# Kernel optimization log

Hardware: AMD Instinct MI355X
Metric: run time of the kernel (lower is better)

## Reference

```python
import jax, jax.numpy as jnp
import numpy as np

# Matches init_kwargs: pc_range=[-54,-54,-5,54,54,3], voxel_size=[0.2,0.2,1.0]
PC_LO = jnp.array([-54.0, -54.0, -5.0], jnp.float32)
PC_HI = jnp.array([54.0, 54.0, 3.0], jnp.float32)
VOX = jnp.array([0.2, 0.2, 1.0], jnp.float32)
NX, NY, NZ = 540, 540, 8          # round((hi-lo)/voxel_size), x,y,z order
NV = NX * NY * NZ                  # dense voxel count (2,332,800)


def setup_inputs() -> dict:
    key = jax.random.key(0)
    B, N = 4, 300000
    k1, k2 = jax.random.split(key)
    center = (PC_LO + PC_HI) / 2.0
    half = (PC_HI - PC_LO) / 2.0 * 1.05
    xyz = center + (jax.random.uniform(k1, (B, N, 3), jnp.float32) * 2.0 - 1.0) * half
    feats = jax.random.normal(k2, (B, N, 2), jnp.float32)
    points = jnp.concatenate([xyz, feats], axis=-1)  # [B, N, 5]
    return {"points": points}


def reference(points):
    """Dynamic voxelization: range filter + quantize + scatter-mean per voxel.

    torch's data-dependent `unique` + compaction is not jit-shapeable, so the
    per-voxel means are returned on the dense [NV, F] grid (occupied voxels are
    those with counts > 0); the math per occupied voxel is identical to the
    original scatter_mean over unique coords.
    """
    grid_max = jnp.array([NX - 1, NY - 1, NZ - 1], jnp.int32)

    def voxelize(pts):  # pts: [N, 5]
        xyz = pts[:, :3]
        keep = jnp.all((xyz >= PC_LO) & (xyz <= PC_HI), axis=1)  # [N]
        # coords in (z, y, x) order in the original; compute (x,y,z) then linearize as z-major
        c = jnp.floor((xyz - PC_LO) / VOX).astype(jnp.int32)
        c = jnp.clip(c, 0, grid_max)  # boundary points (x == hi) map to last cell
        lin = (c[:, 2] * NY + c[:, 1]) * NX + c[:, 0]  # [N]
        lin = jnp.where(keep, lin, NV)  # dropped points -> dummy segment
        pts_m = jnp.where(keep[:, None], pts, 0.0)
        sums = jax.ops.segment_sum(pts_m, lin, num_segments=NV + 1)[:NV]            # [NV, 5]
        cnts = jax.ops.segment_sum(keep.astype(pts.dtype), lin, num_segments=NV + 1)[:NV]  # [NV]
        means = sums / jnp.maximum(cnts, 1.0)[:, None]
        return means, cnts

    voxels, counts = jax.vmap(voxelize)(points)  # [B, NV, 5], [B, NV]
    shape_np = jnp.array([NX, NY, NZ], jnp.int32)
    return voxels, counts, shape_np
```

## Files before the change

kernel.cpp:

```cpp
#include <hip/hip_runtime.h>


#define NX_ 540
#define NY_ 540
#define NZ_ 8
#define NV_ (NX_ * NY_ * NZ_)
#define B_ 4
#define N_ 300000
#define BN_ (B_ * N_)
#define NVB_ (B_ * NV_)


__global__ __launch_bounds__(256) void voxel_build(
    const float* __restrict__ pts,
    int* __restrict__ head,
    int* __restrict__ nxt)
{
    int g = blockIdx.x * blockDim.x + threadIdx.x;
    if (g >= BN_) return;

    const float* p = pts + (size_t)g * 5;
    float x = p[0];
    float y = p[1];
    float z = p[2];

    bool keep = (x >= -54.0f) & (x <= 54.0f) &
                (y >= -54.0f) & (y <= 54.0f) &
                (z >= -5.0f)  & (z <= 3.0f);
    if (!keep) return;

    int cx = (int)floorf((x + 54.0f) * 5.0f);
    int cy = (int)floorf((y + 54.0f) * 5.0f);
    int cz = (int)floorf(z + 5.0f);
    cx = min(max(cx, 0), NX_ - 1);
    cy = min(max(cy, 0), NY_ - 1);
    cz = min(max(cz, 0), NZ_ - 1);

    int lin = (cz * NY_ + cy) * NX_ + cx;
    int b = g / N_;
    int vox = b * NV_ + lin;

    int old = atomicExch(&head[vox], g);
    nxt[g] = old;
}


__global__ __launch_bounds__(256) void voxel_output4(
    const int* __restrict__ head,
    const int* __restrict__ nxt,
    const float* __restrict__ pts,
    float* __restrict__ means,
    float* __restrict__ cnts,
    float* __restrict__ shape_out)
{
    int t = blockIdx.x * blockDim.x + threadIdx.x;
    if (t == 0) {
        shape_out[0] = 540.0f;
        shape_out[1] = 540.0f;
        shape_out[2] = 8.0f;
    }
    int v0 = t * 4;
    if (v0 >= NVB_) return;

    int4 h4 = *(const int4*)(head + v0);
    int hh[4] = {h4.x, h4.y, h4.z, h4.w};

    float o[20];
    float cf[4];

    #pragma unroll
    for (int j = 0; j < 4; j++) {
        int i = hh[j];
        float s0 = 0.f, s1 = 0.f, s2 = 0.f, s3 = 0.f, s4 = 0.f;
        int c = 0;
        while (i >= 0) {
            const float* p = pts + (size_t)i * 5;
            s0 += p[0]; s1 += p[1]; s2 += p[2]; s3 += p[3]; s4 += p[4];
            c++;
            i = nxt[i];
        }
        float d = (float)max(c, 1);
        o[j * 5 + 0] = s0 / d;
        o[j * 5 + 1] = s1 / d;
        o[j * 5 + 2] = s2 / d;
        o[j * 5 + 3] = s3 / d;
        o[j * 5 + 4] = s4 / d;
        cf[j] = (float)c;
    }

    float* mb = means + (size_t)v0 * 5;
    #pragma unroll
    for (int k = 0; k < 5; k++) {
        *(float4*)(mb + k * 4) = make_float4(o[k*4+0], o[k*4+1], o[k*4+2], o[k*4+3]);
    }
    *(float4*)(cnts + v0) = make_float4(cf[0], cf[1], cf[2], cf[3]);
}


__global__ __launch_bounds__(256) void voxel_scatter(
    const float* __restrict__ pts,
    float* __restrict__ sums,
    float* __restrict__ cnts)
{
    int g = blockIdx.x * blockDim.x + threadIdx.x;
    if (g >= BN_) return;
    const float* p = pts + (size_t)g * 5;
    float x = p[0], y = p[1], z = p[2], f0 = p[3], f1 = p[4];
    bool keep = (x >= -54.0f) & (x <= 54.0f) &
                (y >= -54.0f) & (y <= 54.0f) &
                (z >= -5.0f)  & (z <= 3.0f);
    if (!keep) return;
    int cx = (int)floorf((x + 54.0f) * 5.0f);
    int cy = (int)floorf((y + 54.0f) * 5.0f);
    int cz = (int)floorf(z + 5.0f);
    cx = min(max(cx, 0), NX_ - 1);
    cy = min(max(cy, 0), NY_ - 1);
    cz = min(max(cz, 0), NZ_ - 1);
    int lin = (cz * NY_ + cy) * NX_ + cx;
    int b = g / N_;
    size_t vox = (size_t)b * NV_ + (size_t)lin;
    size_t base = vox * 5;
    atomicAdd(&sums[base + 0], x);
    atomicAdd(&sums[base + 1], y);
    atomicAdd(&sums[base + 2], z);
    atomicAdd(&sums[base + 3], f0);
    atomicAdd(&sums[base + 4], f1);
    atomicAdd(&cnts[vox], 1.0f);
}

__global__ __launch_bounds__(256) void voxel_finalize(
    float* __restrict__ sums,
    const float* __restrict__ cnts,
    float* __restrict__ shape_out)
{
    size_t idx = (size_t)blockIdx.x * blockDim.x + threadIdx.x;
    if (idx == 0) {
        shape_out[0] = 540.0f;
        shape_out[1] = 540.0f;
        shape_out[2] = 8.0f;
    }
    if (idx >= (size_t)NVB_) return;
    float c = cnts[idx];
    if (c > 0.0f) {
        size_t base = idx * 5;
        sums[base + 0] /= c;
        sums[base + 1] /= c;
        sums[base + 2] /= c;
        sums[base + 3] /= c;
        sums[base + 4] /= c;
    }
}


extern "C" void kernel_launch(void* const* d_in, const int* in_sizes, int n_in,
                              void* d_out, int out_size, void* d_ws, size_t ws_size,
                              hipStream_t stream) {
    const float* points = (const float*)d_in[0];
    float* out = (float*)d_out;

    float* means     = out;
    float* cnts      = out + (size_t)NVB_ * 5;
    float* shape_out = out + (size_t)NVB_ * 6;

    const size_t head_bytes = (size_t)NVB_ * 4;
    const size_t nxt_bytes  = (size_t)BN_ * 4;
    const size_t need = head_bytes + nxt_bytes;

    if (ws_size >= need) {
        int* head = (int*)d_ws;
        int* nxt  = (int*)((char*)d_ws + head_bytes);

        hipMemsetAsync(head, 0xFF, head_bytes, stream);

        voxel_build<<<(BN_ + 255) / 256, 256, 0, stream>>>(points, head, nxt);

        int threads = NVB_ / 4;
        voxel_output4<<<(threads + 255) / 256, 256, 0, stream>>>(
            head, nxt, points, means, cnts, shape_out);
    } else {
        hipMemsetAsync(d_out, 0, (size_t)out_size * sizeof(float), stream);
        voxel_scatter<<<(BN_ + 255) / 256, 256, 0, stream>>>(points, means, cnts);
        voxel_finalize<<<(NVB_ + 255) / 256, 256, 0, stream>>>(means, cnts, shape_out);
    }
}
```

Measured before the change: 333.0 us.

## Pack point data and next-link into 32-byte nodes; interleave list walks

The build kernel now writes each kept point's five values plus its next-link into one aligned 32-byte node, so the gather kernel follows one contiguous node per step instead of a strided point read plus a separate next-array read. The output kernel also walks its four voxel lists in lockstep, so loads from independent chains can be in flight at the same time. The cost is a larger workspace and extra writes in the build kernel, plus some divergence when list lengths differ.

```diff
diff --git a/kernel.cpp b/kernel.cpp
--- a/kernel.cpp
+++ b/kernel.cpp
@@ -14,15 +14,17 @@
 __global__ __launch_bounds__(256) void voxel_build(
     const float* __restrict__ pts,
     int* __restrict__ head,
-    int* __restrict__ nxt)
+    float* __restrict__ nodes)
 {
     int g = blockIdx.x * blockDim.x + threadIdx.x;
     if (g >= BN_) return;
 
     const float* p = pts + (size_t)g * 5;
-    float x = p[0];
-    float y = p[1];
-    float z = p[2];
+    float x  = p[0];
+    float y  = p[1];
+    float z  = p[2];
+    float f0 = p[3];
+    float f1 = p[4];
 
     bool keep = (x >= -54.0f) & (x <= 54.0f) &
                 (y >= -54.0f) & (y <= 54.0f) &
@@ -40,15 +42,18 @@
     int b = g / N_;
     int vox = b * NV_ + lin;
 
+    float* nb = nodes + (size_t)g * 8;
+    *(float4*)nb = make_float4(x, y, z, f0);
+
     int old = atomicExch(&head[vox], g);
-    nxt[g] = old;
+
+    *(float4*)(nb + 4) = make_float4(f1, __int_as_float(old), 0.0f, 0.0f);
 }
 
 
 __global__ __launch_bounds__(256) void voxel_output4(
     const int* __restrict__ head,
-    const int* __restrict__ nxt,
-    const float* __restrict__ pts,
+    const float* __restrict__ nodes,
     float* __restrict__ means,
     float* __restrict__ cnts,
     float* __restrict__ shape_out)
@@ -63,29 +68,49 @@
     if (v0 >= NVB_) return;
 
     int4 h4 = *(const int4*)(head + v0);
-    int hh[4] = {h4.x, h4.y, h4.z, h4.w};
+    int idx[4] = {h4.x, h4.y, h4.z, h4.w};
+
+    float s[4][5];
+    int   c[4];
+    #pragma unroll
+    for (int j = 0; j < 4; j++) {
+        s[j][0] = s[j][1] = s[j][2] = s[j][3] = s[j][4] = 0.f;
+        c[j] = 0;
+    }
+
+    while ((idx[0] | idx[1] | idx[2] | idx[3]) >= 0 ||
+           idx[0] >= 0 || idx[1] >= 0 || idx[2] >= 0 || idx[3] >= 0) {
+        float4 a[4], b[4];
+        #pragma unroll
+        for (int j = 0; j < 4; j++) {
+            if (idx[j] >= 0) {
+                const float* nb = nodes + (size_t)idx[j] * 8;
+                a[j] = *(const float4*)nb;
+                b[j] = *(const float4*)(nb + 4);
+            }
+        }
+        #pragma unroll
+        for (int j = 0; j < 4; j++) {
+            if (idx[j] >= 0) {
+                s[j][0] += a[j].x; s[j][1] += a[j].y; s[j][2] += a[j].z;
+                s[j][3] += a[j].w; s[j][4] += b[j].x;
+                c[j]++;
+                idx[j] = __float_as_int(b[j].y);
+            }
+        }
+    }
 
     float o[20];
     float cf[4];
-
     #pragma unroll
     for (int j = 0; j < 4; j++) {
-        int i = hh[j];
-        float s0 = 0.f, s1 = 0.f, s2 = 0.f, s3 = 0.f, s4 = 0.f;
-        int c = 0;
-        while (i >= 0) {
-            const float* p = pts + (size_t)i * 5;
-            s0 += p[0]; s1 += p[1]; s2 += p[2]; s3 += p[3]; s4 += p[4];
-            c++;
-            i = nxt[i];
-        }
-        float d = (float)max(c, 1);
-        o[j * 5 + 0] = s0 / d;
-        o[j * 5 + 1] = s1 / d;
-        o[j * 5 + 2] = s2 / d;
-        o[j * 5 + 3] = s3 / d;
-        o[j * 5 + 4] = s4 / d;
-        cf[j] = (float)c;
+        float d = (float)max(c[j], 1);
+        o[j * 5 + 0] = s[j][0] / d;
+        o[j * 5 + 1] = s[j][1] / d;
+        o[j * 5 + 2] = s[j][2] / d;
+        o[j * 5 + 3] = s[j][3] / d;
+        o[j * 5 + 4] = s[j][4] / d;
+        cf[j] = (float)c[j];
     }
 
     float* mb = means + (size_t)v0 * 5;
@@ -163,22 +188,22 @@
     float* shape_out = out + (size_t)NVB_ * 6;
 
     const size_t head_bytes = (size_t)NVB_ * 4;
-    const size_t nxt_bytes  = (size_t)BN_ * 4;
-    const size_t need = head_bytes + nxt_bytes;
+    const size_t node_bytes = (size_t)BN_ * 32;
+    const size_t need = head_bytes + node_bytes;
 
     if (ws_size >= need) {
-        int* head = (int*)d_ws;
-        int* nxt  = (int*)((char*)d_ws + head_bytes);
-
-        hipMemsetAsync(head, 0xFF, head_bytes, stream);
-
-        voxel_build<<<(BN_ + 255) / 256, 256, 0, stream>>>(points, head, nxt);
+        int*   head  = (int*)d_ws;
+        float* nodes = (float*)((char*)d_ws + head_bytes);
+
+        (void)hipMemsetAsync(head, 0xFF, head_bytes, stream);
+
+        voxel_build<<<(BN_ + 255) / 256, 256, 0, stream>>>(points, head, nodes);
 
         int threads = NVB_ / 4;
         voxel_output4<<<(threads + 255) / 256, 256, 0, stream>>>(
-            head, nxt, points, means, cnts, shape_out);
+            head, nodes, means, cnts, shape_out);
     } else {
-        hipMemsetAsync(d_out, 0, (size_t)out_size * sizeof(float), stream);
+        (void)hipMemsetAsync(d_out, 0, (size_t)out_size * sizeof(float), stream);
         voxel_scatter<<<(BN_ + 255) / 256, 256, 0, stream>>>(points, means, cnts);
         voxel_finalize<<<(NVB_ + 255) / 256, 256, 0, stream>>>(means, cnts, shape_out);
     }
```

Result: no change. 339.6 us (+2.0%).
